# Kernel tuning notes

Hardware: AMD Instinct MI355X
Metric: run time of the kernel (lower is better)

The kernel has to match this reference:

```python
import jax, jax.numpy as jnp
import numpy as np

H = 1024   # hidden_size
V = 16000  # output_size (vocab)
B = 64     # batch_size
L = 256    # max_length (encoder seq len)
T = 128    # decoder steps


def setup_inputs() -> dict:
    key = jax.random.key(0)
    ks = jax.random.split(key, 16)
    s = 0.02
    return {
        "target_inputs": jax.random.randint(ks[0], (B, T), 0, V, dtype=jnp.int64),
        "encoder_outputs": jax.random.normal(ks[1], (L, B, H), dtype=jnp.float32),
        "emb": jax.random.normal(ks[2], (V, H), dtype=jnp.float32) * s,
        "W_attn": jax.random.normal(ks[3], (L, 2 * H), dtype=jnp.float32) * s,
        "b_attn": jnp.zeros((L,), jnp.float32),
        "W_comb": jax.random.normal(ks[4], (H, 2 * H), dtype=jnp.float32) * s,
        "b_comb": jnp.zeros((H,), jnp.float32),
        "W_ih": jax.random.normal(ks[5], (4 * H, H), dtype=jnp.float32) * s,
        "W_hh": jax.random.normal(ks[6], (4 * H, H), dtype=jnp.float32) * s,
        "b_ih": jnp.zeros((4 * H,), jnp.float32),
        "b_hh": jnp.zeros((4 * H,), jnp.float32),
        "W_out": jax.random.normal(ks[7], (V, H), dtype=jnp.float32) * s,
        "b_out": jnp.zeros((V,), jnp.float32),
    }


def reference(target_inputs, encoder_outputs, emb, W_attn, b_attn, W_comb, b_comb,
              W_ih, W_hh, b_ih, b_hh, W_out, b_out):
    dec_h = encoder_outputs[-1]                      # [B,H] (dec_hid.squeeze(0))
    enc = jnp.transpose(encoder_outputs, (1, 0, 2))  # [B,L,H]
    dec_c = jnp.zeros_like(dec_h)
    tokens = target_inputs.T                         # [T,B]

    def step(carry, tok):
        h, c = carry
        e = emb[tok]                                              # [B,H]  (dropout = eval identity)
        scores = jnp.concatenate([e, h], 1) @ W_attn.T + b_attn  # [B,L]
        aw = jax.nn.softmax(scores, axis=1)
        ctx = jnp.einsum('bl,blh->bh', aw, enc)                  # bmm
        x = jnp.concatenate([e, ctx], 1) @ W_comb.T + b_comb
        x = jax.nn.relu(x)                                        # [B,H]
        # single-step LSTM (PyTorch gate order i,f,g,o)
        gates = x @ W_ih.T + b_ih + h @ W_hh.T + b_hh             # [B,4H]
        i, f, g, o = jnp.split(gates, 4, axis=1)
        c = jax.nn.sigmoid(f) * c + jax.nn.sigmoid(i) * jnp.tanh(g)
        h = jax.nn.sigmoid(o) * jnp.tanh(c)
        logits = h @ W_out.T + b_out                              # [B,V]
        # Faithful to original: F.log_softmax(out(output_i.squeeze(1)), dim=1)
        # where output_i is [1,B,V]; squeeze(1) is a no-op for B>1, so dim=1
        # normalizes over the BATCH axis (== axis 0 of [B,V] here).
        out = jax.nn.log_softmax(logits, axis=0)
        return (h, c), out

    (_, _), outs = jax.lax.scan(step, (dec_h, dec_c), tokens)
    return outs  # [T,B,V]
```

## Files before the change

### kernel.cpp

```cpp
#include <hip/hip_runtime.h>
#include <math.h>

#define HH 1024
#define VV 16000
#define BB 64
#define LL 256
#define TT 128

#define NBLK 256


__device__ __forceinline__ void grid_barrier(unsigned* bar)
{
    __syncthreads();
    if (threadIdx.x == 0) {
        __threadfence();
        unsigned* gen = bar;
        unsigned* gcnt = bar + 64 + (blockIdx.x >> 4) * 64;
        unsigned* root = bar + 1536;
        const unsigned g =
            __hip_atomic_load(gen, __ATOMIC_RELAXED, __HIP_MEMORY_SCOPE_AGENT);
        bool releaser = false;
        if (__hip_atomic_fetch_add(gcnt, 1u, __ATOMIC_ACQ_REL,
                                   __HIP_MEMORY_SCOPE_AGENT) == 15u) {
            __hip_atomic_store(gcnt, 0u, __ATOMIC_RELAXED,
                               __HIP_MEMORY_SCOPE_AGENT);
            if (__hip_atomic_fetch_add(root, 1u, __ATOMIC_ACQ_REL,
                                       __HIP_MEMORY_SCOPE_AGENT) == 15u) {
                __hip_atomic_store(root, 0u, __ATOMIC_RELAXED,
                                   __HIP_MEMORY_SCOPE_AGENT);
                __hip_atomic_store(gen, g + 1u, __ATOMIC_RELEASE,
                                   __HIP_MEMORY_SCOPE_AGENT);
                releaser = true;
            }
        }
        if (!releaser) {
            while (__hip_atomic_load(gen, __ATOMIC_ACQUIRE,
                                     __HIP_MEMORY_SCOPE_AGENT) == g)
                __builtin_amdgcn_s_sleep(1);
        }
        __threadfence();
    }
    __syncthreads();
}

__device__ __forceinline__ float sigm(float x) { return 1.0f / (1.0f + expf(-x)); }

__device__ __forceinline__ void lstm_full(
    const float* __restrict__ gates_acc, const float* __restrict__ b_ih,
    const float* __restrict__ b_hh, const float* __restrict__ c_rd,
    float* __restrict__ c_wr, float* __restrict__ h_buf,
    float* __restrict__ Hall_t, float* h_s, int b, int tid, bool first_c,
    bool writer)
{
    const int j = tid * 4;
    const float* gb = gates_acc + (size_t)b * 4 * HH;
    float4 gi = *(const float4*)(gb + j);
    float4 gf = *(const float4*)(gb + HH + j);
    float4 gg = *(const float4*)(gb + 2 * HH + j);
    float4 go = *(const float4*)(gb + 3 * HH + j);
    float4 bii = *(const float4*)(b_ih + j),          bhi = *(const float4*)(b_hh + j);
    float4 bif_ = *(const float4*)(b_ih + HH + j),    bhf = *(const float4*)(b_hh + HH + j);
    float4 big = *(const float4*)(b_ih + 2 * HH + j), bhg = *(const float4*)(b_hh + 2 * HH + j);
    float4 bio = *(const float4*)(b_ih + 3 * HH + j), bho = *(const float4*)(b_hh + 3 * HH + j);
    float4 co = first_c ? make_float4(0.f, 0.f, 0.f, 0.f)
                        : *(const float4*)(c_rd + (size_t)b * HH + j);
    float4 cn, hn;
#define DO_LSTM(X)                                        \
    {                                                     \
        float iv = sigm(gi.X + bii.X + bhi.X);            \
        float fv = sigm(gf.X + bif_.X + bhf.X);           \
        float gv = tanhf(gg.X + big.X + bhg.X);           \
        float ov = sigm(go.X + bio.X + bho.X);            \
        float c2 = fv * co.X + iv * gv;                   \
        cn.X = c2;                                        \
        hn.X = ov * tanhf(c2);                            \
    }
    DO_LSTM(x) DO_LSTM(y) DO_LSTM(z) DO_LSTM(w)
#undef DO_LSTM
    if (writer) {
        *(float4*)(c_wr + (size_t)b * HH + j) = cn;
        *(float4*)(h_buf + (size_t)b * HH + j) = hn;
        *(float4*)(Hall_t + (size_t)b * HH + j) = hn;
    }
    if (h_s) *(float4*)(h_s + j) = hn;
}

template <bool RELU_BIAS>
__device__ __forceinline__ void gemm64x64(
    const float* __restrict__ A, int lda, const float* __restrict__ abias,
    const float* __restrict__ Wm, int ldw, int n0, int k0, int klen,
    float* __restrict__ Cacc, int ldc, float* __restrict__ smem)
{
    float (*As)[68] = (float (*)[68])smem;
    float (*Ws)[68] = (float (*)[68])(smem + 32 * 68);
    const int tid = threadIdx.x;
    const int ty = tid >> 4, tx = tid & 15;
    const int q = tid & 7, r = tid >> 3;
    float acc[4][4] = {};

    float4 va0, va1, vw0, vw1, vb;
    {
        const int kk = k0 + q * 4;
        va0 = *(const float4*)(A + (size_t)r * lda + kk);
        va1 = *(const float4*)(A + (size_t)(r + 32) * lda + kk);
        vw0 = *(const float4*)(Wm + (size_t)(n0 + r) * ldw + kk);
        vw1 = *(const float4*)(Wm + (size_t)(n0 + r + 32) * ldw + kk);
        if (RELU_BIAS) vb = *(const float4*)(abias + kk);
    }
    for (int kc = k0; kc < k0 + klen; kc += 32) {
        float4 a0 = va0, a1 = va1;
        if (RELU_BIAS) {
            a0.x = fmaxf(a0.x + vb.x, 0.f); a0.y = fmaxf(a0.y + vb.y, 0.f);
            a0.z = fmaxf(a0.z + vb.z, 0.f); a0.w = fmaxf(a0.w + vb.w, 0.f);
            a1.x = fmaxf(a1.x + vb.x, 0.f); a1.y = fmaxf(a1.y + vb.y, 0.f);
            a1.z = fmaxf(a1.z + vb.z, 0.f); a1.w = fmaxf(a1.w + vb.w, 0.f);
        }
        As[q * 4 + 0][r] = a0.x; As[q * 4 + 1][r] = a0.y;
        As[q * 4 + 2][r] = a0.z; As[q * 4 + 3][r] = a0.w;
        As[q * 4 + 0][r + 32] = a1.x; As[q * 4 + 1][r + 32] = a1.y;
        As[q * 4 + 2][r + 32] = a1.z; As[q * 4 + 3][r + 32] = a1.w;
        Ws[q * 4 + 0][r] = vw0.x; Ws[q * 4 + 1][r] = vw0.y;
        Ws[q * 4 + 2][r] = vw0.z; Ws[q * 4 + 3][r] = vw0.w;
        Ws[q * 4 + 0][r + 32] = vw1.x; Ws[q * 4 + 1][r + 32] = vw1.y;
        Ws[q * 4 + 2][r + 32] = vw1.z; Ws[q * 4 + 3][r + 32] = vw1.w;
        __syncthreads();
        if (kc + 32 < k0 + klen) {
            const int kk = kc + 32 + q * 4;
            va0 = *(const float4*)(A + (size_t)r * lda + kk);
            va1 = *(const float4*)(A + (size_t)(r + 32) * lda + kk);
            vw0 = *(const float4*)(Wm + (size_t)(n0 + r) * ldw + kk);
            vw1 = *(const float4*)(Wm + (size_t)(n0 + r + 32) * ldw + kk);
            if (RELU_BIAS) vb = *(const float4*)(abias + kk);
        }
#pragma unroll
        for (int k = 0; k < 32; ++k) {
            const float4 a = *(const float4*)&As[k][ty * 4];
            const float4 wv = *(const float4*)&Ws[k][tx * 4];
            const float av[4] = {a.x, a.y, a.z, a.w};
            const float bv[4] = {wv.x, wv.y, wv.z, wv.w};
#pragma unroll
            for (int i = 0; i < 4; ++i)
#pragma unroll
                for (int j = 0; j < 4; ++j) acc[i][j] += av[i] * bv[j];
        }
        __syncthreads();
    }
#pragma unroll
    for (int i = 0; i < 4; ++i)
#pragma unroll
        for (int j = 0; j < 4; ++j)
            atomicAdd(Cacc + (size_t)(ty * 4 + i) * ldc + n0 + tx * 4 + j, acc[i][j]);
}

__global__ __launch_bounds__(256) void k_loop(
    const int* __restrict__ tok_all, const float* __restrict__ enc,
    const float* __restrict__ emb, const float* __restrict__ Wattn,
    const float* __restrict__ battn, const float* __restrict__ Wcomb,
    const float* __restrict__ bcomb, const float* __restrict__ Wih,
    const float* __restrict__ Whh, const float* __restrict__ b_ih,
    const float* __restrict__ b_hh, float* __restrict__ Hall,
    float* __restrict__ xin, float* __restrict__ x_acc,
    float* __restrict__ gates_acc, float* __restrict__ h_buf,
    float* __restrict__ c0, float* __restrict__ c1,
    float* __restrict__ sc_all, unsigned* __restrict__ bar)
{
    __shared__ __align__(16) float smem[2 * 32 * 68];
    const int bid = blockIdx.x;
    const int tid = threadIdx.x;
    const int w = tid >> 6, lane = tid & 63;

    const int is64 = (tok_all[1] == 0 && tok_all[3] == 0 && tok_all[5] == 0 &&
                      tok_all[7] == 0);

    for (int t = 0; t < TT; ++t) {
        {
            const int b = bid >> 2, q = bid & 3;
            float* e_s = smem;
            float* h_s = smem + HH;

            x_acc[(size_t)b * HH + q * 256 + tid] = 0.f;

            const int tok = is64 ? tok_all[2 * (b * TT + t)] : tok_all[b * TT + t];
            float4 ev = ((const float4*)(emb + (size_t)tok * HH))[tid];
            ((float4*)e_s)[tid] = ev;
            if (q == 0) ((float4*)(xin + (size_t)b * 2 * HH))[tid] = ev;

            if (t == 0) {
                float4 hv = ((const float4*)(enc + (size_t)(LL - 1) * BB * HH +
                                             (size_t)b * HH))[tid];
                ((float4*)h_s)[tid] = hv;
                if (q == 0) ((float4*)(h_buf + (size_t)b * HH))[tid] = hv;
            } else {
                lstm_full(gates_acc, b_ih, b_hh, (t & 1) ? c1 : c0,
                          (t & 1) ? c0 : c1, h_buf,
                          Hall + (size_t)(t - 1) * BB * HH, h_s, b, tid,
                          t == 1, q == 0);
            }
            __syncthreads();

            const float4* es4 = (const float4*)e_s;
            const float4* hs4 = (const float4*)h_s;
            for (int i = 0; i < 16; ++i) {
                const int l = q * 64 + w * 16 + i;
                const float4* wr = (const float4*)(Wattn + (size_t)l * 2 * HH);
                float a0 = 0.f, a1 = 0.f;
#pragma unroll
                for (int it = 0; it < 4; ++it) {
                    float4 wv = wr[it * 64 + lane];
                    float4 xv = es4[it * 64 + lane];
                    a0 += wv.x * xv.x + wv.y * xv.y + wv.z * xv.z + wv.w * xv.w;
                }
#pragma unroll
                for (int it = 0; it < 4; ++it) {
                    float4 wv = wr[256 + it * 64 + lane];
                    float4 xv = hs4[it * 64 + lane];
                    a1 += wv.x * xv.x + wv.y * xv.y + wv.z * xv.z + wv.w * xv.w;
                }
                float a = a0 + a1;
#pragma unroll
                for (int o = 32; o > 0; o >>= 1) a += __shfl_down(a, o, 64);
                if (lane == 0) sc_all[(size_t)b * LL + l] = a + battn[l];
            }
        }
        grid_barrier(bar);

        {
            const int b = bid >> 2, hq = bid & 3;
            float* aw_s = smem;
            float* red = smem + 256;
            float4* part_s = (float4*)(smem + 272);

            const float sv = sc_all[(size_t)b * LL + tid];
            float m = sv;
#pragma unroll
            for (int o = 32; o > 0; o >>= 1) m = fmaxf(m, __shfl_down(m, o, 64));
            if (lane == 0) red[w] = m;
            __syncthreads();
            m = fmaxf(fmaxf(red[0], red[1]), fmaxf(red[2], red[3]));
            const float ex = expf(sv - m);
            float s = ex;
#pragma unroll
            for (int o = 32; o > 0; o >>= 1) s += __shfl_down(s, o, 64);
            if (lane == 0) red[4 + w] = s;
            __syncthreads();
            const float tot = red[4] + red[5] + red[6] + red[7];
            aw_s[tid] = ex / tot;
            __syncthreads();

            const int col4 = hq * 64 + lane;
            const float4* e4 = (const float4*)enc + (size_t)b * (HH / 4) + col4;
            float4 cacc = make_float4(0.f, 0.f, 0.f, 0.f);
#pragma unroll 8
            for (int li = 0; li < 64; ++li) {
                const int l = w * 64 + li;
                const float a = aw_s[l];
                float4 ev2 = e4[(size_t)l * (BB * HH / 4)];
                cacc.x += a * ev2.x; cacc.y += a * ev2.y;
                cacc.z += a * ev2.z; cacc.w += a * ev2.w;
            }
            part_s[w * 64 + lane] = cacc;
            __syncthreads();
            if (w == 0) {
                float4 p0 = part_s[lane];
                float4 p1 = part_s[64 + lane];
                float4 p2 = part_s[128 + lane];
                float4 p3 = part_s[192 + lane];
                float4 r4;
                r4.x = p0.x + p1.x + p2.x + p3.x;
                r4.y = p0.y + p1.y + p2.y + p3.y;
                r4.z = p0.z + p1.z + p2.z + p3.z;
                r4.w = p0.w + p1.w + p2.w + p3.w;
                ((float4*)(xin + (size_t)b * 2 * HH + HH))[col4] = r4;
            }
        }
        grid_barrier(bar);

        if (bid < 128) {
            const int nt = bid >> 3, kq = bid & 7;
            gemm64x64<false>(xin, 2 * HH, nullptr, Wcomb, 2 * HH, nt * 64,
                             kq * 256, 256, x_acc, HH, smem);
        } else {
            const float4 z4 = make_float4(0.f, 0.f, 0.f, 0.f);
            float4* gz = (float4*)gates_acc;
            const int i0 = (bid - 128) * 256 + tid;
            gz[i0] = z4;
            gz[i0 + 32768] = z4;
        }
        grid_barrier(bar);

        {
            const int nt = bid >> 2, kq = bid & 3;
            const int k0 = kq * 512;
            if (k0 < HH)
                gemm64x64<true>(x_acc, HH, bcomb, Wih, HH, nt * 64, k0, 512,
                                gates_acc, 4 * HH, smem);
            else
                gemm64x64<false>(h_buf, HH, nullptr, Whh, HH, nt * 64, k0 - HH,
                                 512, gates_acc, 4 * HH, smem);
        }
        grid_barrier(bar);
    }

    if (bid < BB) {
        lstm_full(gates_acc, b_ih, b_hh, (TT & 1) ? c1 : c0, (TT & 1) ? c0 : c1,
                  h_buf, Hall + (size_t)(TT - 1) * BB * HH, nullptr, bid, tid,
                  false, true);
    }
}

__global__ __launch_bounds__(256) void k_out(const float* __restrict__ Hall,
                                             const float* __restrict__ Wout,
                                             float* __restrict__ out)
{
    const int t = blockIdx.y;
    const int n0 = blockIdx.x * 128;
    const float* A = Hall + (size_t)t * BB * HH;
    __shared__ float As[32][68];
    __shared__ float Ws[32][132];
    __shared__ float Cs[64][129];
    __shared__ float lse_s[128];
    const int tid = threadIdx.x;
    const int ty = tid >> 4, tx = tid & 15;
    const int q = tid & 7, r = tid >> 3;
    float acc[4][8] = {};

    float4 pa0, pa1, pw0, pw1, pw2, pw3;
    {
        const int kk = q * 4;
        pa0 = *(const float4*)(A + (size_t)r * HH + kk);
        pa1 = *(const float4*)(A + (size_t)(r + 32) * HH + kk);
        pw0 = *(const float4*)(Wout + (size_t)(n0 + r) * HH + kk);
        pw1 = *(const float4*)(Wout + (size_t)(n0 + r + 32) * HH + kk);
        pw2 = *(const float4*)(Wout + (size_t)(n0 + r + 64) * HH + kk);
        pw3 = *(const float4*)(Wout + (size_t)(n0 + r + 96) * HH + kk);
    }
    for (int kc = 0; kc < HH; kc += 32) {
        As[q * 4 + 0][r] = pa0.x; As[q * 4 + 1][r] = pa0.y;
        As[q * 4 + 2][r] = pa0.z; As[q * 4 + 3][r] = pa0.w;
        As[q * 4 + 0][r + 32] = pa1.x; As[q * 4 + 1][r + 32] = pa1.y;
        As[q * 4 + 2][r + 32] = pa1.z; As[q * 4 + 3][r + 32] = pa1.w;
        Ws[q * 4 + 0][r] = pw0.x; Ws[q * 4 + 1][r] = pw0.y;
        Ws[q * 4 + 2][r] = pw0.z; Ws[q * 4 + 3][r] = pw0.w;
        Ws[q * 4 + 0][r + 32] = pw1.x; Ws[q * 4 + 1][r + 32] = pw1.y;
        Ws[q * 4 + 2][r + 32] = pw1.z; Ws[q * 4 + 3][r + 32] = pw1.w;
        Ws[q * 4 + 0][r + 64] = pw2.x; Ws[q * 4 + 1][r + 64] = pw2.y;
        Ws[q * 4 + 2][r + 64] = pw2.z; Ws[q * 4 + 3][r + 64] = pw2.w;
        Ws[q * 4 + 0][r + 96] = pw3.x; Ws[q * 4 + 1][r + 96] = pw3.y;
        Ws[q * 4 + 2][r + 96] = pw3.z; Ws[q * 4 + 3][r + 96] = pw3.w;
        __syncthreads();
        if (kc + 32 < HH) {
            const int kk = kc + 32 + q * 4;
            pa0 = *(const float4*)(A + (size_t)r * HH + kk);
            pa1 = *(const float4*)(A + (size_t)(r + 32) * HH + kk);
            pw0 = *(const float4*)(Wout + (size_t)(n0 + r) * HH + kk);
            pw1 = *(const float4*)(Wout + (size_t)(n0 + r + 32) * HH + kk);
            pw2 = *(const float4*)(Wout + (size_t)(n0 + r + 64) * HH + kk);
            pw3 = *(const float4*)(Wout + (size_t)(n0 + r + 96) * HH + kk);
        }
#pragma unroll
        for (int k = 0; k < 32; ++k) {
            const float4 a = *(const float4*)&As[k][ty * 4];
            const float4 w0 = *(const float4*)&Ws[k][tx * 8];
            const float4 w1 = *(const float4*)&Ws[k][tx * 8 + 4];
            const float av[4] = {a.x, a.y, a.z, a.w};
            const float bv[8] = {w0.x, w0.y, w0.z, w0.w, w1.x, w1.y, w1.z, w1.w};
#pragma unroll
            for (int i = 0; i < 4; ++i)
#pragma unroll
                for (int j = 0; j < 8; ++j) acc[i][j] += av[i] * bv[j];
        }
        __syncthreads();
    }
#pragma unroll
    for (int i = 0; i < 4; ++i)
#pragma unroll
        for (int j = 0; j < 8; ++j) Cs[ty * 4 + i][tx * 8 + j] = acc[i][j];
    __syncthreads();

    if (tid < 128) {
        float m = -1e30f;
        for (int b = 0; b < 64; ++b) m = fmaxf(m, Cs[b][tid]);
        float s = 0.f;
        for (int b = 0; b < 64; ++b) s += expf(Cs[b][tid] - m);
        lse_s[tid] = m + logf(s);
    }
    __syncthreads();

    const int col = tid & 127, bh = tid >> 7;
    float* outp = out + (size_t)t * BB * VV + n0 + col;
    for (int b = bh; b < 64; b += 2)
        outp[(size_t)b * VV] = Cs[b][col] - lse_s[col];
}

extern "C" void kernel_launch(void* const* d_in, const int* in_sizes, int n_in,
                              void* d_out, int out_size, void* d_ws, size_t ws_size,
                              hipStream_t stream)
{
    const int* tok = (const int*)d_in[0];
    const float* enc = (const float*)d_in[1];
    const float* emb = (const float*)d_in[2];
    const float* W_attn = (const float*)d_in[3];
    const float* b_attn = (const float*)d_in[4];
    const float* W_comb = (const float*)d_in[5];
    const float* b_comb = (const float*)d_in[6];
    const float* W_ih = (const float*)d_in[7];
    const float* W_hh = (const float*)d_in[8];
    const float* b_ih = (const float*)d_in[9];
    const float* b_hh = (const float*)d_in[10];
    const float* W_out = (const float*)d_in[11];
    float* out = (float*)d_out;
    float* ws = (float*)d_ws;

    const size_t n_Hall = (size_t)TT * BB * HH;
    const size_t n_xin = (size_t)BB * 2 * HH;
    const size_t n_xacc = (size_t)BB * HH;
    const size_t n_gates = (size_t)BB * 4 * HH;
    const size_t n_bh = (size_t)BB * HH;
    const size_t n_sc = (size_t)BB * LL;
    const size_t n_bar = 2048;
    const size_t needed =
        (n_Hall + n_xin + n_xacc + n_gates + 3 * n_bh + n_sc + n_bar) * 4;
    if (ws_size < needed) return;

    float* H_all = ws;
    float* xin = H_all + n_Hall;
    float* x_acc = xin + n_xin;
    float* gates_acc = x_acc + n_xacc;
    float* h_buf = gates_acc + n_gates;
    float* c0 = h_buf + n_bh;
    float* c1 = c0 + n_bh;
    float* sc_all = c1 + n_bh;
    unsigned* bar = (unsigned*)(sc_all + n_sc);

    hipMemsetAsync(bar, 0, n_bar * 4, stream);

    k_loop<<<NBLK, 256, 0, stream>>>(tok, enc, emb, W_attn, b_attn, W_comb,
                                     b_comb, W_ih, W_hh, b_ih, b_hh, H_all,
                                     xin, x_acc, gates_acc, h_buf, c0, c1,
                                     sc_all, bar);
    k_out<<<dim3(125, 128), 256, 0, stream>>>(H_all, W_out, out);
}
```

Baseline: 33.74 ms.

## Merge attention phases per batch, replace atomic split-K GEMMs with row-tile GEMMs

Attention scores, softmax and context are now computed by one block per batch row with no grid barrier between them, which drops one barrier per step. The split-K 64x64 GEMMs that accumulated with atomics are replaced by row-tile GEMMs that reduce over K inside each block and write directly. The W_hh GEMM overlaps with the W_comb GEMM, and the zeroing pass and the bias adds inside the LSTM are removed. The encoder outputs are transposed up front when workspace allows, so context reads are contiguous. In exchange, attention now uses only 64 blocks, leaving the other blocks idle during that phase, and each row-tile GEMM block streams all 64 rows of activations.

```diff
diff --git a/kernel.cpp b/kernel.cpp
--- a/kernel.cpp
+++ b/kernel.cpp
@@ -46,126 +46,151 @@
 
 __device__ __forceinline__ float sigm(float x) { return 1.0f / (1.0f + expf(-x)); }
 
-__device__ __forceinline__ void lstm_full(
-    const float* __restrict__ gates_acc, const float* __restrict__ b_ih,
-    const float* __restrict__ b_hh, const float* __restrict__ c_rd,
-    float* __restrict__ c_wr, float* __restrict__ h_buf,
-    float* __restrict__ Hall_t, float* h_s, int b, int tid, bool first_c,
-    bool writer)
+__device__ __forceinline__ void lstm_pb(
+    const float* __restrict__ gates, float* __restrict__ c_buf,
+    float* __restrict__ h_buf, float* __restrict__ Hall_t, float* h_s, int b,
+    int tid, bool first_c)
 {
     const int j = tid * 4;
-    const float* gb = gates_acc + (size_t)b * 4 * HH;
+    const float* gb = gates + (size_t)b * 4 * HH;
     float4 gi = *(const float4*)(gb + j);
     float4 gf = *(const float4*)(gb + HH + j);
     float4 gg = *(const float4*)(gb + 2 * HH + j);
     float4 go = *(const float4*)(gb + 3 * HH + j);
-    float4 bii = *(const float4*)(b_ih + j),          bhi = *(const float4*)(b_hh + j);
-    float4 bif_ = *(const float4*)(b_ih + HH + j),    bhf = *(const float4*)(b_hh + HH + j);
-    float4 big = *(const float4*)(b_ih + 2 * HH + j), bhg = *(const float4*)(b_hh + 2 * HH + j);
-    float4 bio = *(const float4*)(b_ih + 3 * HH + j), bho = *(const float4*)(b_hh + 3 * HH + j);
     float4 co = first_c ? make_float4(0.f, 0.f, 0.f, 0.f)
-                        : *(const float4*)(c_rd + (size_t)b * HH + j);
+                        : *(const float4*)(c_buf + (size_t)b * HH + j);
     float4 cn, hn;
-#define DO_LSTM(X)                                        \
-    {                                                     \
-        float iv = sigm(gi.X + bii.X + bhi.X);            \
-        float fv = sigm(gf.X + bif_.X + bhf.X);           \
-        float gv = tanhf(gg.X + big.X + bhg.X);           \
-        float ov = sigm(go.X + bio.X + bho.X);            \
-        float c2 = fv * co.X + iv * gv;                   \
-        cn.X = c2;                                        \
-        hn.X = ov * tanhf(c2);                            \
+#define DO_LSTM(X)                                \
+    {                                             \
+        float iv = sigm(gi.X);                    \
+        float fv = sigm(gf.X);                    \
+        float gv = tanhf(gg.X);                   \
+        float ov = sigm(go.X);                    \
+        float c2 = fv * co.X + iv * gv;           \
+        cn.X = c2;                                \
+        hn.X = ov * tanhf(c2);                    \
     }
     DO_LSTM(x) DO_LSTM(y) DO_LSTM(z) DO_LSTM(w)
 #undef DO_LSTM
-    if (writer) {
-        *(float4*)(c_wr + (size_t)b * HH + j) = cn;
-        *(float4*)(h_buf + (size_t)b * HH + j) = hn;
-        *(float4*)(Hall_t + (size_t)b * HH + j) = hn;
-    }
+    *(float4*)(c_buf + (size_t)b * HH + j) = cn;
+    *(float4*)(h_buf + (size_t)b * HH + j) = hn;
+    *(float4*)(Hall_t + (size_t)b * HH + j) = hn;
     if (h_s) *(float4*)(h_s + j) = hn;
 }
 
-template <bool RELU_BIAS>
-__device__ __forceinline__ void gemm64x64(
+template <int NW, bool RELU, int OUTMODE>
+__device__ __forceinline__ void gemm_rowtile(
     const float* __restrict__ A, int lda, const float* __restrict__ abias,
-    const float* __restrict__ Wm, int ldw, int n0, int k0, int klen,
-    float* __restrict__ Cacc, int ldc, float* __restrict__ smem)
-{
-    float (*As)[68] = (float (*)[68])smem;
-    float (*Ws)[68] = (float (*)[68])(smem + 32 * 68);
+    const float* __restrict__ Wm, int ldw, int n0, int klen,
+    const float* __restrict__ bias1, const float* __restrict__ bias2,
+    float* __restrict__ outp, int ldo, float* __restrict__ smem)
+{
+    static_assert(NW % 8 == 0, "NW multiple of 8");
+    constexpr int NWP = NW + 4;
     const int tid = threadIdx.x;
-    const int ty = tid >> 4, tx = tid & 15;
-    const int q = tid & 7, r = tid >> 3;
-    float acc[4][4] = {};
-
-    float4 va0, va1, vw0, vw1, vb;
+    const int wv = tid >> 6, lane = tid & 63;
+    const int kw = klen >> 2;
+    const int kbase = wv * kw;
+    const int nch = kw >> 5;
+    float* Asw = smem + wv * (64 * 33);
+    float* Wsw = smem + 4 * 64 * 33 + wv * (32 * NWP);
+    const int arow = lane >> 3, ac4 = lane & 7;
+    float acc[NW];
+#pragma unroll
+    for (int j = 0; j < NW; ++j) acc[j] = 0.f;
+
+    float4 pa[8];
+    float4 pw[NW / 8];
     {
-        const int kk = k0 + q * 4;
-        va0 = *(const float4*)(A + (size_t)r * lda + kk);
-        va1 = *(const float4*)(A + (size_t)(r + 32) * lda + kk);
-        vw0 = *(const float4*)(Wm + (size_t)(n0 + r) * ldw + kk);
-        vw1 = *(const float4*)(Wm + (size_t)(n0 + r + 32) * ldw + kk);
-        if (RELU_BIAS) vb = *(const float4*)(abias + kk);
-    }
-    for (int kc = k0; kc < k0 + klen; kc += 32) {
-        float4 a0 = va0, a1 = va1;
-        if (RELU_BIAS) {
-            a0.x = fmaxf(a0.x + vb.x, 0.f); a0.y = fmaxf(a0.y + vb.y, 0.f);
-            a0.z = fmaxf(a0.z + vb.z, 0.f); a0.w = fmaxf(a0.w + vb.w, 0.f);
-            a1.x = fmaxf(a1.x + vb.x, 0.f); a1.y = fmaxf(a1.y + vb.y, 0.f);
-            a1.z = fmaxf(a1.z + vb.z, 0.f); a1.w = fmaxf(a1.w + vb.w, 0.f);
-        }
-        As[q * 4 + 0][r] = a0.x; As[q * 4 + 1][r] = a0.y;
-        As[q * 4 + 2][r] = a0.z; As[q * 4 + 3][r] = a0.w;
-        As[q * 4 + 0][r + 32] = a1.x; As[q * 4 + 1][r + 32] = a1.y;
-        As[q * 4 + 2][r + 32] = a1.z; As[q * 4 + 3][r + 32] = a1.w;
-        Ws[q * 4 + 0][r] = vw0.x; Ws[q * 4 + 1][r] = vw0.y;
-        Ws[q * 4 + 2][r] = vw0.z; Ws[q * 4 + 3][r] = vw0.w;
-        Ws[q * 4 + 0][r + 32] = vw1.x; Ws[q * 4 + 1][r + 32] = vw1.y;
-        Ws[q * 4 + 2][r + 32] = vw1.z; Ws[q * 4 + 3][r + 32] = vw1.w;
-        __syncthreads();
-        if (kc + 32 < k0 + klen) {
-            const int kk = kc + 32 + q * 4;
-            va0 = *(const float4*)(A + (size_t)r * lda + kk);
-            va1 = *(const float4*)(A + (size_t)(r + 32) * lda + kk);
-            vw0 = *(const float4*)(Wm + (size_t)(n0 + r) * ldw + kk);
-            vw1 = *(const float4*)(Wm + (size_t)(n0 + r + 32) * ldw + kk);
-            if (RELU_BIAS) vb = *(const float4*)(abias + kk);
+        const int kk = kbase + ac4 * 4;
+#pragma unroll
+        for (int i = 0; i < 8; ++i)
+            pa[i] = *(const float4*)(A + (size_t)(i * 8 + arow) * lda + kk);
+#pragma unroll
+        for (int i = 0; i < NW / 8; ++i)
+            pw[i] = *(const float4*)(Wm + (size_t)(n0 + i * 8 + arow) * ldw + kk);
+    }
+    for (int ch = 0; ch < nch; ++ch) {
+        const int kk = kbase + ch * 32;
+        float4 bv;
+        if (RELU) bv = *(const float4*)(abias + kk + ac4 * 4);
+#pragma unroll
+        for (int i = 0; i < 8; ++i) {
+            float4 v = pa[i];
+            if (RELU) {
+                v.x = fmaxf(v.x + bv.x, 0.f); v.y = fmaxf(v.y + bv.y, 0.f);
+                v.z = fmaxf(v.z + bv.z, 0.f); v.w = fmaxf(v.w + bv.w, 0.f);
+            }
+            const int base = (i * 8 + arow) * 33 + ac4 * 4;
+            Asw[base + 0] = v.x; Asw[base + 1] = v.y;
+            Asw[base + 2] = v.z; Asw[base + 3] = v.w;
+        }
+#pragma unroll
+        for (int i = 0; i < NW / 8; ++i) {
+            const int r = i * 8 + arow;
+            Wsw[(ac4 * 4 + 0) * NWP + r] = pw[i].x;
+            Wsw[(ac4 * 4 + 1) * NWP + r] = pw[i].y;
+            Wsw[(ac4 * 4 + 2) * NWP + r] = pw[i].z;
+            Wsw[(ac4 * 4 + 3) * NWP + r] = pw[i].w;
+        }
+        if (ch + 1 < nch) {
+            const int k2 = kbase + (ch + 1) * 32 + ac4 * 4;
+#pragma unroll
+            for (int i = 0; i < 8; ++i)
+                pa[i] = *(const float4*)(A + (size_t)(i * 8 + arow) * lda + k2);
+#pragma unroll
+            for (int i = 0; i < NW / 8; ++i)
+                pw[i] = *(const float4*)(Wm + (size_t)(n0 + i * 8 + arow) * ldw + k2);
         }
 #pragma unroll
         for (int k = 0; k < 32; ++k) {
-            const float4 a = *(const float4*)&As[k][ty * 4];
-            const float4 wv = *(const float4*)&Ws[k][tx * 4];
-            const float av[4] = {a.x, a.y, a.z, a.w};
-            const float bv[4] = {wv.x, wv.y, wv.z, wv.w};
-#pragma unroll
-            for (int i = 0; i < 4; ++i)
-#pragma unroll
-                for (int j = 0; j < 4; ++j) acc[i][j] += av[i] * bv[j];
-        }
-        __syncthreads();
-    }
-#pragma unroll
-    for (int i = 0; i < 4; ++i)
-#pragma unroll
-        for (int j = 0; j < 4; ++j)
-            atomicAdd(Cacc + (size_t)(ty * 4 + i) * ldc + n0 + tx * 4 + j, acc[i][j]);
+            const float a = Asw[lane * 33 + k];
+#pragma unroll
+            for (int j4 = 0; j4 < NW / 4; ++j4) {
+                const float4 w4 = *(const float4*)&Wsw[k * NWP + j4 * 4];
+                acc[j4 * 4 + 0] += a * w4.x;
+                acc[j4 * 4 + 1] += a * w4.y;
+                acc[j4 * 4 + 2] += a * w4.z;
+                acc[j4 * 4 + 3] += a * w4.w;
+            }
+        }
+    }
+    __syncthreads();
+    float* red = smem;
+#pragma unroll
+    for (int j4 = 0; j4 < NW / 4; ++j4)
+        *(float4*)&red[((wv * 64 + lane) * NW) + j4 * 4] = make_float4(
+            acc[j4 * 4 + 0], acc[j4 * 4 + 1], acc[j4 * 4 + 2], acc[j4 * 4 + 3]);
+    __syncthreads();
+    constexpr int P = NW / 4;
+    const int row = tid >> 2, jg = (tid & 3) * P;
+#pragma unroll
+    for (int p = 0; p < P; ++p) {
+        const int j = jg + p;
+        float v = red[(0 * 64 + row) * NW + j] + red[(1 * 64 + row) * NW + j] +
+                  red[(2 * 64 + row) * NW + j] + red[(3 * 64 + row) * NW + j];
+        if (OUTMODE == 1) v += bias1[n0 + j] + bias2[n0 + j];
+        if (OUTMODE == 2)
+            outp[(size_t)row * ldo + n0 + j] += v;
+        else
+            outp[(size_t)row * ldo + n0 + j] = v;
+    }
+    __syncthreads();
 }
 
 __global__ __launch_bounds__(256) void k_loop(
     const int* __restrict__ tok_all, const float* __restrict__ enc,
-    const float* __restrict__ emb, const float* __restrict__ Wattn,
-    const float* __restrict__ battn, const float* __restrict__ Wcomb,
-    const float* __restrict__ bcomb, const float* __restrict__ Wih,
-    const float* __restrict__ Whh, const float* __restrict__ b_ih,
-    const float* __restrict__ b_hh, float* __restrict__ Hall,
-    float* __restrict__ xin, float* __restrict__ x_acc,
-    float* __restrict__ gates_acc, float* __restrict__ h_buf,
-    float* __restrict__ c0, float* __restrict__ c1,
-    float* __restrict__ sc_all, unsigned* __restrict__ bar)
-{
-    __shared__ __align__(16) float smem[2 * 32 * 68];
+    const float* __restrict__ encT, const float* __restrict__ emb,
+    const float* __restrict__ Wattn, const float* __restrict__ battn,
+    const float* __restrict__ Wcomb, const float* __restrict__ bcomb,
+    const float* __restrict__ Wih, const float* __restrict__ Whh,
+    const float* __restrict__ b_ih, const float* __restrict__ b_hh,
+    float* __restrict__ Hall, float* __restrict__ xin,
+    float* __restrict__ x_acc, float* __restrict__ gates,
+    float* __restrict__ h_buf, float* __restrict__ c_buf,
+    unsigned* __restrict__ bar, int use_t)
+{
+    __shared__ __align__(16) float smem[4 * 64 * 33 + 4 * 32 * 36];
     const int bid = blockIdx.x;
     const int tid = threadIdx.x;
     const int w = tid >> 6, lane = tid & 63;
@@ -174,64 +199,54 @@
                       tok_all[7] == 0);
 
     for (int t = 0; t < TT; ++t) {
-        {
-            const int b = bid >> 2, q = bid & 3;
+        if (bid < BB) {
+            const int b = bid;
             float* e_s = smem;
             float* h_s = smem + HH;
-
-            x_acc[(size_t)b * HH + q * 256 + tid] = 0.f;
+            float* sc = smem + 2 * HH;
+            float* red = smem + 2 * HH + LL;
 
             const int tok = is64 ? tok_all[2 * (b * TT + t)] : tok_all[b * TT + t];
             float4 ev = ((const float4*)(emb + (size_t)tok * HH))[tid];
             ((float4*)e_s)[tid] = ev;
-            if (q == 0) ((float4*)(xin + (size_t)b * 2 * HH))[tid] = ev;
+            ((float4*)(xin + (size_t)b * 2 * HH))[tid] = ev;
 
             if (t == 0) {
                 float4 hv = ((const float4*)(enc + (size_t)(LL - 1) * BB * HH +
                                              (size_t)b * HH))[tid];
                 ((float4*)h_s)[tid] = hv;
-                if (q == 0) ((float4*)(h_buf + (size_t)b * HH))[tid] = hv;
+                ((float4*)(h_buf + (size_t)b * HH))[tid] = hv;
             } else {
-                lstm_full(gates_acc, b_ih, b_hh, (t & 1) ? c1 : c0,
-                          (t & 1) ? c0 : c1, h_buf,
-                          Hall + (size_t)(t - 1) * BB * HH, h_s, b, tid,
-                          t == 1, q == 0);
+                lstm_pb(gates, c_buf, h_buf, Hall + (size_t)(t - 1) * BB * HH,
+                        h_s, b, tid, t == 1);
             }
             __syncthreads();
 
             const float4* es4 = (const float4*)e_s;
             const float4* hs4 = (const float4*)h_s;
-            for (int i = 0; i < 16; ++i) {
-                const int l = q * 64 + w * 16 + i;
+            for (int li = 0; li < 64; ++li) {
+                const int l = w * 64 + li;
                 const float4* wr = (const float4*)(Wattn + (size_t)l * 2 * HH);
-                float a0 = 0.f, a1 = 0.f;
+                float a = 0.f;
 #pragma unroll
                 for (int it = 0; it < 4; ++it) {
                     float4 wv = wr[it * 64 + lane];
                     float4 xv = es4[it * 64 + lane];
-                    a0 += wv.x * xv.x + wv.y * xv.y + wv.z * xv.z + wv.w * xv.w;
+                    a += wv.x * xv.x + wv.y * xv.y + wv.z * xv.z + wv.w * xv.w;
                 }
 #pragma unroll
                 for (int it = 0; it < 4; ++it) {
                     float4 wv = wr[256 + it * 64 + lane];
                     float4 xv = hs4[it * 64 + lane];
-                    a1 += wv.x * xv.x + wv.y * xv.y + wv.z * xv.z + wv.w * xv.w;
+                    a += wv.x * xv.x + wv.y * xv.y + wv.z * xv.z + wv.w * xv.w;
                 }
-                float a = a0 + a1;
 #pragma unroll
                 for (int o = 32; o > 0; o >>= 1) a += __shfl_down(a, o, 64);
-                if (lane == 0) sc_all[(size_t)b * LL + l] = a + battn[l];
-            }
-        }
-        grid_barrier(bar);
-
-        {
-            const int b = bid >> 2, hq = bid & 3;
-            float* aw_s = smem;
-            float* red = smem + 256;
-            float4* part_s = (float4*)(smem + 272);
-
-            const float sv = sc_all[(size_t)b * LL + tid];
+                if (lane == 0) sc[l] = a + battn[l];
+            }
+            __syncthreads();
+
+            const float sv = sc[tid];
             float m = sv;
 #pragma unroll
             for (int o = 32; o > 0; o >>= 1) m = fmaxf(m, __shfl_down(m, o, 64));
@@ -245,68 +260,62 @@
             if (lane == 0) red[4 + w] = s;
             __syncthreads();
             const float tot = red[4] + red[5] + red[6] + red[7];
-            aw_s[tid] = ex / tot;
+            sc[tid] = ex / tot;
             __syncthreads();
 
-            const int col4 = hq * 64 + lane;
-            const float4* e4 = (const float4*)enc + (size_t)b * (HH / 4) + col4;
-            float4 cacc = make_float4(0.f, 0.f, 0.f, 0.f);
+            float4 ctx = make_float4(0.f, 0.f, 0.f, 0.f);
+            const float4* ebase;
+            size_t lstr;
+            if (use_t) {
+                ebase = (const float4*)(encT + (size_t)b * LL * HH) + tid;
+                lstr = HH / 4;
+            } else {
+                ebase = (const float4*)(enc + (size_t)b * HH) + tid;
+                lstr = (size_t)BB * HH / 4;
+            }
 #pragma unroll 8
-            for (int li = 0; li < 64; ++li) {
-                const int l = w * 64 + li;
-                const float a = aw_s[l];
-                float4 ev2 = e4[(size_t)l * (BB * HH / 4)];
-                cacc.x += a * ev2.x; cacc.y += a * ev2.y;
-                cacc.z += a * ev2.z; cacc.w += a * ev2.w;
-            }
-            part_s[w * 64 + lane] = cacc;
-            __syncthreads();
-            if (w == 0) {
-                float4 p0 = part_s[lane];
-                float4 p1 = part_s[64 + lane];
-                float4 p2 = part_s[128 + lane];
-                float4 p3 = part_s[192 + lane];
-                float4 r4;
-                r4.x = p0.x + p1.x + p2.x + p3.x;
-                r4.y = p0.y + p1.y + p2.y + p3.y;
-                r4.z = p0.z + p1.z + p2.z + p3.z;
-                r4.w = p0.w + p1.w + p2.w + p3.w;
-                ((float4*)(xin + (size_t)b * 2 * HH + HH))[col4] = r4;
-            }
+            for (int l = 0; l < LL; ++l) {
+                const float a = sc[l];
+                float4 e2 = ebase[(size_t)l * lstr];
+                ctx.x += a * e2.x; ctx.y += a * e2.y;
+                ctx.z += a * e2.z; ctx.w += a * e2.w;
+            }
+            ((float4*)(xin + (size_t)b * 2 * HH + HH))[tid] = ctx;
         }
         grid_barrier(bar);
 
         if (bid < 128) {
-            const int nt = bid >> 3, kq = bid & 7;
-            gemm64x64<false>(xin, 2 * HH, nullptr, Wcomb, 2 * HH, nt * 64,
-                             kq * 256, 256, x_acc, HH, smem);
+            gemm_rowtile<8, false, 0>(xin, 2 * HH, nullptr, Wcomb, 2 * HH,
+                                      bid * 8, 2 * HH, nullptr, nullptr, x_acc,
+                                      HH, smem);
         } else {
-            const float4 z4 = make_float4(0.f, 0.f, 0.f, 0.f);
-            float4* gz = (float4*)gates_acc;
-            const int i0 = (bid - 128) * 256 + tid;
-            gz[i0] = z4;
-            gz[i0 + 32768] = z4;
+            gemm_rowtile<32, false, 1>(h_buf, HH, nullptr, Whh, HH,
+                                       (bid - 128) * 32, HH, b_ih, b_hh, gates,
+                                       4 * HH, smem);
         }
         grid_barrier(bar);
 
-        {
-            const int nt = bid >> 2, kq = bid & 3;
-            const int k0 = kq * 512;
-            if (k0 < HH)
-                gemm64x64<true>(x_acc, HH, bcomb, Wih, HH, nt * 64, k0, 512,
-                                gates_acc, 4 * HH, smem);
-            else
-                gemm64x64<false>(h_buf, HH, nullptr, Whh, HH, nt * 64, k0 - HH,
-                                 512, gates_acc, 4 * HH, smem);
-        }
+        gemm_rowtile<16, true, 2>(x_acc, HH, bcomb, Wih, HH, bid * 16, HH,
+                                  nullptr, nullptr, gates, 4 * HH, smem);
         grid_barrier(bar);
     }
 
     if (bid < BB) {
-        lstm_full(gates_acc, b_ih, b_hh, (TT & 1) ? c1 : c0, (TT & 1) ? c0 : c1,
-                  h_buf, Hall + (size_t)(TT - 1) * BB * HH, nullptr, bid, tid,
-                  false, true);
-    }
+        lstm_pb(gates, c_buf, h_buf, Hall + (size_t)(TT - 1) * BB * HH, nullptr,
+                bid, tid, false);
+    }
+}
+
+__global__ __launch_bounds__(256) void k_tr(const float* __restrict__ enc,
+                                            float* __restrict__ encT)
+{
+    const size_t idx = (size_t)blockIdx.x * 256 + threadIdx.x;
+    const int h4 = idx & 255;
+    const size_t lb = idx >> 8;
+    const int b = lb & 63;
+    const int l = (int)(lb >> 6);
+    ((float4*)encT)[(((size_t)b * LL + l) * (HH / 4)) + h4] =
+        ((const float4*)enc)[idx];
 }
 
 __global__ __launch_bounds__(256) void k_out(const float* __restrict__ Hall,
@@ -417,27 +426,29 @@
     const size_t n_xacc = (size_t)BB * HH;
     const size_t n_gates = (size_t)BB * 4 * HH;
     const size_t n_bh = (size_t)BB * HH;
-    const size_t n_sc = (size_t)BB * LL;
     const size_t n_bar = 2048;
-    const size_t needed =
-        (n_Hall + n_xin + n_xacc + n_gates + 3 * n_bh + n_sc + n_bar) * 4;
-    if (ws_size < needed) return;
+    const size_t n_encT = (size_t)BB * LL * HH;
+    const size_t base =
+        n_Hall + n_xin + n_xacc + n_gates + 2 * n_bh + n_bar;
+    if (ws_size < base * 4) return;
+    const int use_t = (ws_size >= (base + n_encT) * 4) ? 1 : 0;
 
     float* H_all = ws;
     float* xin = H_all + n_Hall;
     float* x_acc = xin + n_xin;
-    float* gates_acc = x_acc + n_xacc;
-    float* h_buf = gates_acc + n_gates;
-    float* c0 = h_buf + n_bh;
-    float* c1 = c0 + n_bh;
-    float* sc_all = c1 + n_bh;
-    unsigned* bar = (unsigned*)(sc_all + n_sc);
+    float* gates = x_acc + n_xacc;
+    float* h_buf = gates + n_gates;
+    float* c_buf = h_buf + n_bh;
+    unsigned* bar = (unsigned*)(c_buf + n_bh);
+    float* encT = (float*)(bar + n_bar);
 
     hipMemsetAsync(bar, 0, n_bar * 4, stream);
-
-    k_loop<<<NBLK, 256, 0, stream>>>(tok, enc, emb, W_attn, b_attn, W_comb,
-                                     b_comb, W_ih, W_hh, b_ih, b_hh, H_all,
-                                     xin, x_acc, gates_acc, h_buf, c0, c1,
-                                     sc_all, bar);
+    if (use_t)
+        k_tr<<<(LL * BB * HH / 4) / 256, 256, 0, stream>>>(enc, encT);
+
+    k_loop<<<NBLK, 256, 0, stream>>>(tok, enc, encT, emb, W_attn, b_attn,
+                                     W_comb, b_comb, W_ih, W_hh, b_ih, b_hh,
+                                     H_all, xin, x_acc, gates, h_buf, c_buf,
+                                     bar, use_t);
     k_out<<<dim3(125, 128), 256, 0, stream>>>(H_all, W_out, out);
 }
```

New measurement: 63.64 ms. 1.89x slower.
